# Kernel optimization log

Measured on AMD Instinct MI355X. Metric: run time of the kernel, lower is better.

## Reference

```python
import jax, jax.numpy as jnp
import numpy as np

N_HEAD = 16
LN_EPS = 1e-5     # torch LayerNorm default
ATTN_EPS = 1e-6   # fast-transformers CausalLinearAttention eps


def layer_norm(x, g, b):
    mu = x.mean(-1, keepdims=True)
    var = ((x - mu) ** 2).mean(-1, keepdims=True)
    return (x - mu) * jax.lax.rsqrt(var + LN_EPS) * g + b


def favor(x, omega):
    # Favor/Performer softmax-kernel features.
    # x: [B,S,H,dh], omega: [dh, m/2] -> phi: [B,S,H,m] with m = 2*(dh//2) = dh
    dh = x.shape[-1]
    m = 2 * omega.shape[-1]
    xs = x * (dh ** -0.25)  # x * sqrt(softmax_temp), softmax_temp = 1/sqrt(dh)
    u = jnp.einsum('bshd,dm->bshm', xs, omega)
    h = 0.5 * jnp.sum(xs * xs, axis=-1, keepdims=True)  # ||x||^2 / 2
    return jnp.concatenate([jnp.exp(u - h), jnp.exp(-u - h)], axis=-1) * (m ** -0.5)


def causal_linear_attention(q, k, v):
    # q,k: [B,S,H,M] feature-mapped; v: [B,S,H,Dv]
    # out[i] = (phiQ_i @ sum_{j<=i} phiK_j v_j^T) / (phiQ_i . sum_{j<=i} phiK_j)
    B, S, H, M = q.shape
    Dv = v.shape[-1]
    qT = jnp.moveaxis(q, 1, 0)  # [S,B,H,M]
    kT = jnp.moveaxis(k, 1, 0)
    vT = jnp.moveaxis(v, 1, 0)  # [S,B,H,Dv]
    S0 = jnp.zeros((B, H, M, Dv), q.dtype)
    z0 = jnp.zeros((B, H, M), q.dtype)

    def step(carry, qkv):
        Sst, zst = carry
        qi, ki, vi = qkv
        Sst = Sst + ki[..., :, None] * vi[..., None, :]  # [B,H,M,Dv]
        zst = zst + ki                                   # [B,H,M]
        num = jnp.einsum('bhm,bhmd->bhd', qi, Sst)
        den = jnp.einsum('bhm,bhm->bh', qi, zst) + ATTN_EPS
        return (Sst, zst), num / den[..., None]

    _, out = jax.lax.scan(step, (S0, z0), (qT, kT, vT))
    return jnp.moveaxis(out, 0, 1)  # [B,S,H,Dv]


def forward(x, Wq, bq, Wk, bk, Wv, bv, Wo, bo, omega,
            ln1_g, ln1_b, ln2_g, ln2_b, W1, bf1, W2, bf2):
    L = Wq.shape[0]
    B, S, D = x.shape
    dh = D // N_HEAD
    out = x
    for l in range(L):  # fixed small layer count
        q = (out @ Wq[l] + bq[l]).reshape(B, S, N_HEAD, dh)
        k = (out @ Wk[l] + bk[l]).reshape(B, S, N_HEAD, dh)
        v = (out @ Wv[l] + bv[l]).reshape(B, S, N_HEAD, dh)
        Qf = favor(q, omega[l])
        Kf = favor(k, omega[l])
        a = causal_linear_attention(Qf, Kf, v).reshape(B, S, D)
        a = a @ Wo[l] + bo[l]
        h = layer_norm(out + a, ln1_g[l], ln1_b[l])          # norm1 (post-norm)
        y = jax.nn.relu(h @ W1[l] + bf1[l]) @ W2[l] + bf2[l]  # FFN
        out = layer_norm(h + y, ln2_g[l], ln2_b[l])          # norm2
    return out


def setup_inputs() -> dict:
    key = jax.random.key(0)
    L, B, S, D, DFF = 3, 2, 1024, 1024, 4096
    dh = D // N_HEAD
    ks = jax.random.split(key, 8)
    g = lambda k, shape: jax.random.normal(k, shape, jnp.float32) * 0.02
    return {
        'x': jax.random.normal(ks[0], (B, S, D), jnp.float32),
        'Wq': g(ks[1], (L, D, D)), 'bq': jnp.zeros((L, D), jnp.float32),
        'Wk': g(ks[2], (L, D, D)), 'bk': jnp.zeros((L, D), jnp.float32),
        'Wv': g(ks[3], (L, D, D)), 'bv': jnp.zeros((L, D), jnp.float32),
        'Wo': g(ks[4], (L, D, D)), 'bo': jnp.zeros((L, D), jnp.float32),
        'omega': jax.random.normal(ks[5], (L, dh, dh // 2), jnp.float32),
        'ln1_g': jnp.ones((L, D), jnp.float32), 'ln1_b': jnp.zeros((L, D), jnp.float32),
        'ln2_g': jnp.ones((L, D), jnp.float32), 'ln2_b': jnp.zeros((L, D), jnp.float32),
        'W1': g(ks[6], (L, D, DFF)), 'bf1': jnp.zeros((L, DFF), jnp.float32),
        'W2': g(ks[7], (L, DFF, D)), 'bf2': jnp.zeros((L, D), jnp.float32),
    }


def reference(x, Wq, bq, Wk, bk, Wv, bv, Wo, bo, omega,
              ln1_g, ln1_b, ln2_g, ln2_b, W1, bf1, W2, bf2):
    return forward(x, Wq, bq, Wk, bk, Wv, bv, Wo, bo, omega,
                   ln1_g, ln1_b, ln2_g, ln2_b, W1, bf1, W2, bf2)
```

## Files before the change

### kernel.cpp

```cpp
#include <hip/hip_runtime.h>

typedef unsigned int u32;
typedef unsigned short u16;
typedef unsigned long long u64;

#define LN_EPS 1e-5f
#define ATTN_EPS 1e-6f

typedef __bf16 bf16x8 __attribute__((ext_vector_type(8)));
typedef short shortx8 __attribute__((ext_vector_type(8)));
typedef float fx4 __attribute__((ext_vector_type(4)));

__device__ __forceinline__ u16 f2bf(float f){
  union{float f; u32 u;} x; x.f = f;
  u32 r = 0x7fffu + ((x.u>>16)&1u);
  return (u16)((x.u + r)>>16);
}
__device__ __forceinline__ float bf2f(u16 u){
  union{u32 u; float f;} x; x.u = ((u32)u)<<16; return x.f;
}
__device__ __forceinline__ bf16x8 ldfrag(const u16* p){
  return __builtin_bit_cast(bf16x8, *(const shortx8*)p);
}

__device__ __forceinline__ void async16(const void* g, void* l){
  typedef const __attribute__((address_space(1))) void gas_t;
  typedef __attribute__((address_space(3))) void las_t;
  __builtin_amdgcn_global_load_lds((gas_t*)(u64)g, (las_t*)(u32)(u64)l, 16, 0, 0);
}

__global__ void detect_kernel(const u16* __restrict__ ln1g, int* __restrict__ flag){
  if (threadIdx.x == 0 && blockIdx.x == 0)
    *flag = (ln1g[0] == 0x3F80u) ? 1 : 0;
}

__global__ __launch_bounds__(256) void cvt_small(
    const void* p0, const void* p1, const void* p2, const void* p3,
    const void* p4, const void* p5, const void* p6, const void* p7,
    const void* p8, const void* p9, const void* p10,
    float* __restrict__ out, const int* __restrict__ flagp)
{
  int i = blockIdx.x*256 + threadIdx.x;
  if (i >= 46080) return;
  const void* src; int off;
  if      (i < 3072)  { src=p0;  off=i; }
  else if (i < 6144)  { src=p1;  off=i-3072; }
  else if (i < 9216)  { src=p2;  off=i-6144; }
  else if (i < 12288) { src=p3;  off=i-9216; }
  else if (i < 18432) { src=p4;  off=i-12288; }
  else if (i < 21504) { src=p5;  off=i-18432; }
  else if (i < 24576) { src=p6;  off=i-21504; }
  else if (i < 27648) { src=p7;  off=i-24576; }
  else if (i < 30720) { src=p8;  off=i-27648; }
  else if (i < 43008) { src=p9;  off=i-30720; }
  else                { src=p10; off=i-43008; }
  float v;
  if (*flagp){ union{u32 u; float f;} x; x.u = ((u32)((const u16*)src)[off])<<16; v = x.f; }
  else v = ((const float*)src)[off];
  out[i] = v;
}

__global__ __launch_bounds__(256) void cvt_x(const void* __restrict__ in, float* __restrict__ out,
                                             u16* __restrict__ outbf, int n, const int* __restrict__ flagp){
  int i = blockIdx.x*256 + threadIdx.x;
  if (i >= n) return;
  float v;
  if (*flagp){ union{u32 u; float f;} x; x.u = ((u32)((const u16*)in)[i])<<16; v = x.f; }
  else v = ((const float*)in)[i];
  out[i] = v;
  outbf[i] = f2bf(v);
}

__global__ __launch_bounds__(256) void transpose_cvt(
    const void* __restrict__ W, size_t eoff, u16* __restrict__ Wt,
    int K, int N, const int* __restrict__ flagp)
{
  __shared__ float s[32][33];
  const int bx = blockIdx.x, by = blockIdx.y;
  const int tid = threadIdx.x;
  const int c = tid & 31, r = tid >> 5;
  const int isbf = *flagp;
#pragma unroll
  for (int i = 0; i < 4; ++i){
    int k = by*32 + r + i*8, n = bx*32 + c;
    size_t idx = eoff + (size_t)k*N + n;
    float v;
    if (isbf){ union{u32 u; float f;} x; x.u = ((u32)((const u16*)W)[idx])<<16; v = x.f; }
    else v = ((const float*)W)[idx];
    s[r + i*8][c] = v;
  }
  __syncthreads();
#pragma unroll
  for (int i = 0; i < 4; ++i){
    int n = bx*32 + r + i*8, k = by*32 + c;
    Wt[(size_t)n*K + k] = f2bf(s[c][r + i*8]);
  }
}

__global__ __launch_bounds__(256) void transpose_cvt4(
    const void* __restrict__ W0, const void* __restrict__ W1,
    const void* __restrict__ W2, const void* __restrict__ W3,
    size_t eoff, u16* __restrict__ Wt, size_t wtz,
    int K, int N, const int* __restrict__ flagp)
{
  __shared__ float s[32][33];
  const int z = blockIdx.z;
  const void* W = (z==0)?W0:((z==1)?W1:((z==2)?W2:W3));
  Wt += (size_t)z * wtz;
  const int bx = blockIdx.x, by = blockIdx.y;
  const int tid = threadIdx.x;
  const int c = tid & 31, r = tid >> 5;
  const int isbf = *flagp;
#pragma unroll
  for (int i = 0; i < 4; ++i){
    int k = by*32 + r + i*8, n = bx*32 + c;
    size_t idx = eoff + (size_t)k*N + n;
    float v;
    if (isbf){ union{u32 u; float f;} x; x.u = ((u32)((const u16*)W)[idx])<<16; v = x.f; }
    else v = ((const float*)W)[idx];
    s[r + i*8][c] = v;
  }
  __syncthreads();
#pragma unroll
  for (int i = 0; i < 4; ++i){
    int n = bx*32 + r + i*8, k = by*32 + c;
    Wt[(size_t)n*K + k] = f2bf(s[c][r + i*8]);
  }
}

__global__ __launch_bounds__(256, 1) void mfma_gemm(
    const u16* __restrict__ A, const u16* __restrict__ W,
    const float* __restrict__ bias,
    float* __restrict__ C, u16* __restrict__ Cbf,
    int N, int Kst, int kstep_z, int klen,
    size_t wz, size_t cz, int bz, int bias_all, int relu)
{
  __shared__ u16 As[3][128*32];
  __shared__ u16 Bs[3][128*32];
  const int z = blockIdx.z;
  W    += (size_t)z * wz;
  bias += (size_t)z * bz;
  if (C) C += (size_t)z * cz;
  const int kbeg = z * kstep_z;
  const int tid = threadIdx.x;
  const int lane = tid & 63, wid = tid >> 6;
  const int row0 = blockIdx.y * 128, col0 = blockIdx.x * 128;

  const int ar0 = tid >> 2,        ae0 = (tid & 3) << 3;
  const int ar1 = (256+tid) >> 2,  ae1 = (tid & 3) << 3;
  const u16* gA0 = A + (size_t)(row0 + ar0)*Kst + kbeg + ae0;
  const u16* gA1 = A + (size_t)(row0 + ar1)*Kst + kbeg + ae1;
  const u16* gB0 = W + (size_t)(col0 + ar0)*Kst + kbeg + ae0;
  const u16* gB1 = W + (size_t)(col0 + ar1)*Kst + kbeg + ae1;

  const int iters = klen >> 5;
#pragma unroll
  for (int s = 0; s < 2; ++s){
    const int ko = s*32;
    async16(gA0 + ko, &As[s][tid*8]);
    async16(gA1 + ko, &As[s][2048 + tid*8]);
    async16(gB0 + ko, &Bs[s][tid*8]);
    async16(gB1 + ko, &Bs[s][2048 + tid*8]);
  }

  const int quad = lane >> 4, l16 = lane & 15;
  const int wr = (wid >> 1) * 64, wc = (wid & 1) * 64;
  fx4 acc[4][4] = {};

  for (int it = 0; it < iters; ++it){
    const int cur = it % 3;
    __builtin_amdgcn_s_waitcnt(0x0F74);
    __builtin_amdgcn_s_barrier();
    {
      const int nx   = (it + 2 < iters) ? (it + 2) : (iters - 1);
      const int nbuf = (it + 2) % 3;
      const int ko = nx*32;
      async16(gA0 + ko, &As[nbuf][tid*8]);
      async16(gA1 + ko, &As[nbuf][2048 + tid*8]);
      async16(gB0 + ko, &Bs[nbuf][tid*8]);
      async16(gB1 + ko, &Bs[nbuf][2048 + tid*8]);
    }
    bf16x8 af[4], bfr[4];
#pragma unroll
    for (int t = 0; t < 4; ++t)
      af[t] = ldfrag(&As[cur][(wr + t*16 + l16)*32 + quad*8]);
#pragma unroll
    for (int u = 0; u < 4; ++u)
      bfr[u] = ldfrag(&Bs[cur][(wc + u*16 + l16)*32 + quad*8]);
#pragma unroll
    for (int t = 0; t < 4; ++t)
#pragma unroll
      for (int u = 0; u < 4; ++u)
        acc[t][u] = __builtin_amdgcn_mfma_f32_16x16x32_bf16(af[t], bfr[u], acc[t][u], 0, 0, 0);
  }
  __builtin_amdgcn_s_waitcnt(0x0F70);

  const int r0 = quad * 4;
#pragma unroll
  for (int u = 0; u < 4; ++u){
    const int col = col0 + wc + u*16 + l16;
    const float bv = (bias_all || z == 0) ? bias[col] : 0.f;
#pragma unroll
    for (int t = 0; t < 4; ++t){
      const int rowb = row0 + wr + t*16 + r0;
#pragma unroll
      for (int r = 0; r < 4; ++r){
        float v = acc[t][u][r] + bv;
        if (relu) v = fmaxf(v, 0.f);
        if (C)   C[(size_t)(rowb + r)*N + col] = v;
        if (Cbf) Cbf[(size_t)(rowb + r)*N + col] = f2bf(v);
      }
    }
  }
}

__global__ __launch_bounds__(256) void favor_kernel(
    float* __restrict__ Q, float* __restrict__ Kp, const float* __restrict__ omega,
    u16* __restrict__ Qb, u16* __restrict__ Kb)
{
  __shared__ float sh[4][64];
  __shared__ float sho[64][32];
  int tid = threadIdx.x;
  for (int i = tid; i < 2048; i += 256)
    sho[i>>5][i&31] = omega[i];
  int wv = tid >> 6, lane = tid & 63;
  int th = blockIdx.x*4 + wv;
  size_t base = (size_t)(th >> 4) * 1024 + (size_t)(th & 15) * 64;
  int jm = lane & 31;
  float sgn = (lane < 32) ? 1.f : -1.f;
  for (int w = 0; w < 2; ++w){
    float* p = w ? Kp : Q;
    float xs = p[base + lane] * 0.35355339059327373f;
    __syncthreads();
    sh[wv][lane] = xs;
    __syncthreads();
    float u = 0.f, hh = 0.f;
#pragma unroll
    for (int d = 0; d < 64; ++d){
      float xv = sh[wv][d];
      u  = fmaf(xv, sho[d][jm], u);
      hh = fmaf(xv, xv, hh);
    }
    float phi = expf(sgn*u - 0.5f*hh) * 0.125f;
    if (w) p[base + lane] = phi;
    (w ? Kb : Qb)[base + lane] = f2bf(phi);
  }
}

__global__ __launch_bounds__(256) void chunk_kv(
    const float* __restrict__ Kf, const float* __restrict__ V,
    float* __restrict__ KV, float* __restrict__ Ksum)
{
  __shared__ float Ks[64][64];
  __shared__ float Vs[64][64];
  int blk = blockIdx.x;
  int c = blk & 15, h = (blk >> 4) & 15, b = blk >> 8;
  int tid = threadIdx.x;
  for (int i = tid; i < 1024; i += 256){
    int j = i >> 4, m4 = (i & 15) << 2;
    size_t src = ((size_t)(b*1024 + c*64 + j)*16 + h)*64 + m4;
    *(float4*)&Ks[j][m4] = *(const float4*)&Kf[src];
    *(float4*)&Vs[j][m4] = *(const float4*)&V[src];
  }
  __syncthreads();
  int m = tid & 63, dg = tid >> 6;
  float acc[16] = {0.f};
  for (int j = 0; j < 64; ++j){
    float kv = Ks[j][m];
#pragma unroll
    for (int di = 0; di < 16; ++di)
      acc[di] = fmaf(Vs[j][dg*16+di], kv, acc[di]);
  }
  size_t outb = (size_t)blk * 4096;
#pragma unroll
  for (int di = 0; di < 16; ++di)
    KV[outb + (size_t)(dg*16+di)*64 + m] = acc[di];
  if (tid < 64){
    float s = 0.f;
    for (int j = 0; j < 64; ++j) s += Ks[j][tid];
    Ksum[(size_t)blk*64 + tid] = s;
  }
}

__global__ __launch_bounds__(256) void chunk_scan(float* __restrict__ KV, float* __restrict__ Ksum)
{
  int blk = blockIdx.x;
  int bh = blk >> 4, ec = blk & 15;
  int e = ec*256 + threadIdx.x;
  size_t base = (size_t)bh * 65536 + e;
  float run = 0.f;
  for (int c = 0; c < 16; ++c){
    size_t idx = base + (size_t)c*4096;
    float t = KV[idx]; KV[idx] = run; run += t;
  }
  if (ec == 0 && threadIdx.x < 64){
    size_t kb = (size_t)bh * 1024 + threadIdx.x;
    float rz = 0.f;
    for (int c = 0; c < 16; ++c){
      size_t idx = kb + c*64;
      float t = Ksum[idx]; Ksum[idx] = rz; rz += t;
    }
  }
}

__global__ __launch_bounds__(256) void attn_kernel(
    const u16* __restrict__ Qbf, const u16* __restrict__ Kbf,
    const float* __restrict__ V, const float* __restrict__ KVt,
    const float* __restrict__ Ksum, u16* __restrict__ Outbf)
{
  __shared__ u16 Qs[64][72];
  __shared__ u16 Ks[64][72];
  __shared__ u16 Ss[64][72];
  __shared__ u16 Vt[64][72];
  __shared__ u16 Pt[64][72];
  __shared__ float Vrow[64][68];
  __shared__ float densum[64];

  const int blk = blockIdx.x;
  const int c = blk & 15, h = (blk >> 4) & 15, b = blk >> 8;
  const int tid = threadIdx.x;
  const int lane = tid & 63, w = tid >> 6;
  const int quad = lane >> 4, l16 = lane & 15;
  const int t0 = b*1024 + c*64;

  {
    const int r = tid >> 2, q4 = (tid & 3) << 4;
    size_t g = (size_t)(t0 + r)*1024 + h*64 + q4;
    *(uint4*)&Qs[r][q4]   = *(const uint4*)(Qbf + g);
    *(uint4*)&Qs[r][q4+8] = *(const uint4*)(Qbf + g + 8);
    *(uint4*)&Ks[r][q4]   = *(const uint4*)(Kbf + g);
    *(uint4*)&Ks[r][q4+8] = *(const uint4*)(Kbf + g + 8);
    const float* vg = V + g;
    *(float4*)&Vrow[r][q4+0]  = *(const float4*)(vg+0);
    *(float4*)&Vrow[r][q4+4]  = *(const float4*)(vg+4);
    *(float4*)&Vrow[r][q4+8]  = *(const float4*)(vg+8);
    *(float4*)&Vrow[r][q4+12] = *(const float4*)(vg+12);
    const float* pg = KVt + (size_t)blk*4096 + r*64 + q4;
    u16 tmp[16];
#pragma unroll
    for (int j = 0; j < 16; ++j) tmp[j] = f2bf(pg[j]);
    *(uint4*)&Pt[r][q4]   = *(uint4*)&tmp[0];
    *(uint4*)&Pt[r][q4+8] = *(uint4*)&tmp[8];
  }
  __syncthreads();
  {
    const int d = tid >> 2, j16 = (tid & 3) << 4;
    u16 tmp[16];
#pragma unroll
    for (int j = 0; j < 16; ++j) tmp[j] = f2bf(Vrow[j16+j][d]);
    *(uint4*)&Vt[d][j16]   = *(uint4*)&tmp[0];
    *(uint4*)&Vt[d][j16+8] = *(uint4*)&tmp[8];
  }

  const int iw0 = w*16;
  bf16x8 aq0 = ldfrag(&Qs[iw0+l16][quad*8]);
  bf16x8 aq1 = ldfrag(&Qs[iw0+l16][32+quad*8]);
  fx4 sacc[4];
#pragma unroll
  for (int u = 0; u < 4; ++u){
    sacc[u] = (fx4){0.f,0.f,0.f,0.f};
    bf16x8 b0 = ldfrag(&Ks[u*16+l16][quad*8]);
    bf16x8 b1 = ldfrag(&Ks[u*16+l16][32+quad*8]);
    sacc[u] = __builtin_amdgcn_mfma_f32_16x16x32_bf16(aq0, b0, sacc[u], 0, 0, 0);
    sacc[u] = __builtin_amdgcn_mfma_f32_16x16x32_bf16(aq1, b1, sacc[u], 0, 0, 0);
  }
  float rs[4] = {0.f,0.f,0.f,0.f};
#pragma unroll
  for (int u = 0; u < 4; ++u){
    const int jl = u*16 + l16;
#pragma unroll
    for (int r = 0; r < 4; ++r){
      const int il = iw0 + quad*4 + r;
      float v = (jl <= il) ? sacc[u][r] : 0.f;
      rs[r] += v;
      Ss[il][jl] = f2bf(v);
    }
  }
#pragma unroll
  for (int off = 1; off < 16; off <<= 1){
#pragma unroll
    for (int r = 0; r < 4; ++r) rs[r] += __shfl_xor(rs[r], off);
  }
  if (l16 == 0){
#pragma unroll
    for (int r = 0; r < 4; ++r) densum[iw0 + quad*4 + r] = rs[r];
  }
  __syncthreads();

  {
    const int row = iw0 + l16;
    const float* zp = Ksum + (size_t)blk*64;
    float dp = 0.f;
#pragma unroll
    for (int m = 0; m < 16; ++m){
      const int mm = quad*16 + m;
      dp = fmaf(bf2f(Qs[row][mm]), zp[mm], dp);
    }
    dp += __shfl_xor(dp, 16);
    dp += __shfl_xor(dp, 32);
    if (quad == 0) densum[row] = densum[row] + dp + ATTN_EPS;
  }
  __syncthreads();

  bf16x8 as0 = ldfrag(&Ss[iw0+l16][quad*8]);
  bf16x8 as1 = ldfrag(&Ss[iw0+l16][32+quad*8]);
  fx4 oacc[4];
#pragma unroll
  for (int u = 0; u < 4; ++u){
    const int d0 = u*16;
    oacc[u] = (fx4){0.f,0.f,0.f,0.f};
    oacc[u] = __builtin_amdgcn_mfma_f32_16x16x32_bf16(as0, ldfrag(&Vt[d0+l16][quad*8]),    oacc[u], 0,0,0);
    oacc[u] = __builtin_amdgcn_mfma_f32_16x16x32_bf16(as1, ldfrag(&Vt[d0+l16][32+quad*8]), oacc[u], 0,0,0);
    oacc[u] = __builtin_amdgcn_mfma_f32_16x16x32_bf16(aq0, ldfrag(&Pt[d0+l16][quad*8]),    oacc[u], 0,0,0);
    oacc[u] = __builtin_amdgcn_mfma_f32_16x16x32_bf16(aq1, ldfrag(&Pt[d0+l16][32+quad*8]), oacc[u], 0,0,0);
  }
#pragma unroll
  for (int u = 0; u < 4; ++u){
    const int d = u*16 + l16;
#pragma unroll
    for (int r = 0; r < 4; ++r){
      const int il = iw0 + quad*4 + r;
      const float o = oacc[u][r] / densum[il];
      Outbf[(size_t)(t0 + il)*1024 + h*64 + d] = f2bf(o);
    }
  }
}

__global__ __launch_bounds__(256) void resid_ln(
    const float* __restrict__ X, const float* __restrict__ Y0, const float* __restrict__ Y1,
    const float* __restrict__ g, const float* __restrict__ b,
    float* __restrict__ Dst, u16* __restrict__ DstBf,
    void* __restrict__ OutPtr, const int* __restrict__ flagp)
{
  __shared__ float rs[4], rss[4];
  int row = blockIdx.x, tid = threadIdx.x;
  int lane = tid & 63, wv = tid >> 6;
  size_t base = (size_t)row * 1024;
  int c = tid << 2;
  float4 xv = *(const float4*)&X[base + c];
  float4 y0 = *(const float4*)&Y0[base + c];
  float4 y1 = *(const float4*)&Y1[base + c];
  float v0 = xv.x+y0.x+y1.x, v1 = xv.y+y0.y+y1.y, v2 = xv.z+y0.z+y1.z, v3 = xv.w+y0.w+y1.w;
  float s = v0+v1+v2+v3;
  float ss = v0*v0+v1*v1+v2*v2+v3*v3;
  for (int off = 32; off; off >>= 1){
    s  += __shfl_down(s, off);
    ss += __shfl_down(ss, off);
  }
  if (lane == 0){ rs[wv] = s; rss[wv] = ss; }
  __syncthreads();
  float S  = rs[0]+rs[1]+rs[2]+rs[3];
  float SS = rss[0]+rss[1]+rss[2]+rss[3];
  float mu = S * (1.f/1024.f);
  float var = SS * (1.f/1024.f) - mu*mu;
  float rinv = rsqrtf(var + LN_EPS);
  float4 gv = *(const float4*)(g + c);
  float4 bb = *(const float4*)(b + c);
  float o0 = (v0-mu)*rinv*gv.x + bb.x;
  float o1 = (v1-mu)*rinv*gv.y + bb.y;
  float o2 = (v2-mu)*rinv*gv.z + bb.z;
  float o3 = (v3-mu)*rinv*gv.w + bb.w;
  *(float4*)&Dst[base + c] = make_float4(o0,o1,o2,o3);
  uint2 ob;
  ob.x = (u32)f2bf(o0) | ((u32)f2bf(o1) << 16);
  ob.y = (u32)f2bf(o2) | ((u32)f2bf(o3) << 16);
  *(uint2*)(DstBf + base + c) = ob;
  if (OutPtr){
    if (*flagp){
      *(uint2*)((u16*)OutPtr + base + c) = ob;
    } else {
      *(float4*)((float*)OutPtr + base + c) = make_float4(o0,o1,o2,o3);
    }
  }
}

extern "C" void kernel_launch(void* const* d_in, const int* in_sizes, int n_in,
                              void* d_out, int out_size, void* d_ws, size_t ws_size,
                              hipStream_t stream)
{
  (void)in_sizes; (void)n_in; (void)out_size; (void)ws_size;

  float* ws   = (float*)d_ws;
  float* bufA = ws;
  float* bufQ = bufA + 2097152;
  float* bufK = bufQ + 2097152;
  float* bufV = bufK + 2097152;
  float* KV   = bufV + 2097152;
  float* Ks   = KV   + 2097152;
  float* smallP = Ks + 32768;
  float* pend = smallP + 46080;
  int* flag = (int*)pend;
  u16* abf  = (u16*)(pend + 4);
  u16* hbf  = abf  + 2097152;
  u16* t1bf = hbf  + 2097152;
  u16* fbf  = t1bf + 2097152;
  u16* Wt   = fbf  + 8388608;
  u16* qpbf = Wt   + 4194304;
  u16* kpbf = qpbf + 2097152;

  float* bqF  = smallP + 0;
  float* boF  = smallP + 9216;
  float* omF  = smallP + 12288;
  float* l1gF = smallP + 18432;
  float* l1bF = smallP + 21504;
  float* l2gF = smallP + 24576;
  float* l2bF = smallP + 27648;
  float* bf1F = smallP + 30720;
  float* bf2F = smallP + 43008;

  detect_kernel<<<1, 64, 0, stream>>>((const u16*)d_in[10], flag);
  cvt_small<<<180, 256, 0, stream>>>(d_in[2], d_in[4], d_in[6], d_in[8], d_in[9],
                                     d_in[10], d_in[11], d_in[12], d_in[13],
                                     d_in[15], d_in[17], smallP, flag);
  cvt_x<<<8192, 256, 0, stream>>>(d_in[0], bufA, abf, 2097152, flag);

  dim3 tQKVO(32, 32, 4);
  dim3 tF1(128, 32);
  dim3 tF2(32, 128);
  dim3 gQKV(8, 16, 3);
  dim3 gO(8, 16, 2);
  dim3 gF1(32, 16, 1);
  dim3 gF2(8, 16, 2);

  for (int l = 0; l < 3; ++l){
    size_t offD = (size_t)l * 1048576;
    size_t offF = (size_t)l * 4194304;

    transpose_cvt4<<<tQKVO, 256, 0, stream>>>(d_in[1], d_in[3], d_in[5], d_in[7],
                                              offD, Wt, 1048576, 1024, 1024, flag);

    mfma_gemm<<<gQKV, 256, 0, stream>>>(abf, Wt, bqF + l*1024, bufQ, (u16*)nullptr,
                                        1024, 1024, 0, 1024,
                                        1048576, 2097152, 3072, 1, 0);
    favor_kernel<<<8192, 256, 0, stream>>>(bufQ, bufK, omF + l*2048, qpbf, kpbf);
    chunk_kv<<<512, 256, 0, stream>>>(bufK, bufV, KV, Ks);
    chunk_scan<<<512, 256, 0, stream>>>(KV, Ks);
    attn_kernel<<<512, 256, 0, stream>>>(qpbf, kpbf, bufV, KV, Ks, t1bf);

    mfma_gemm<<<gO, 256, 0, stream>>>(t1bf, Wt + 3145728, boF + l*1024, bufQ, (u16*)nullptr,
                                      1024, 1024, 512, 512,
                                      0, 4194304, 0, 0, 0);
    resid_ln<<<2048, 256, 0, stream>>>(bufA, bufQ, bufV, l1gF + l*1024, l1bF + l*1024,
                                       bufK, hbf, nullptr, flag);

    transpose_cvt<<<tF1, 256, 0, stream>>>(d_in[14], offF, Wt, 1024, 4096, flag);
    mfma_gemm<<<gF1, 256, 0, stream>>>(hbf, Wt, bf1F + l*4096, (float*)nullptr, fbf,
                                       4096, 1024, 0, 1024,
                                       0, 0, 0, 1, 1);

    transpose_cvt<<<tF2, 256, 0, stream>>>(d_in[16], offF, Wt, 4096, 1024, flag);
    mfma_gemm<<<gF2, 256, 0, stream>>>(fbf, Wt, bf2F + l*1024, bufQ, (u16*)nullptr,
                                       1024, 4096, 2048, 2048,
                                       0, 4194304, 0, 0, 0);

    resid_ln<<<2048, 256, 0, stream>>>(bufK, bufQ, bufV, l2gF + l*1024, l2bF + l*1024,
                                       bufA, abf, (l == 2) ? d_out : nullptr, flag);
  }
}
```

Before: 800.4 us.

## Deepen GEMM pipeline, remap blocks across XCDs, split-K by four for O/FFN2

The GEMM's shared-memory ring grows from three to four stages, with prefetch three tiles ahead and a matching waitcnt. Block indices are remapped so neighbouring column tiles spread across the eight XCDs. The output and FFN2 GEMMs now split K four ways into a new partial buffer, and the residual LayerNorm sums all four partials. This aims to hide more load latency and put more blocks on the device, at the cost of more shared memory per block and extra partial-buffer traffic.

Result: slower. 856.3 us (+7.0%).

```diff
diff --git a/kernel.cpp b/kernel.cpp
--- a/kernel.cpp
+++ b/kernel.cpp
@@ -135,8 +135,8 @@
     int N, int Kst, int kstep_z, int klen,
     size_t wz, size_t cz, int bz, int bias_all, int relu)
 {
-  __shared__ u16 As[3][128*32];
-  __shared__ u16 Bs[3][128*32];
+  __shared__ u16 As[4][128*32];
+  __shared__ u16 Bs[4][128*32];
   const int z = blockIdx.z;
   W    += (size_t)z * wz;
   bias += (size_t)z * bz;
@@ -144,7 +144,11 @@
   const int kbeg = z * kstep_z;
   const int tid = threadIdx.x;
   const int lane = tid & 63, wid = tid >> 6;
-  const int row0 = blockIdx.y * 128, col0 = blockIdx.x * 128;
+
+  const int flat = blockIdx.y * gridDim.x + blockIdx.x;
+  const int xcd = flat & 7, sblk = flat >> 3;
+  const int by = sblk & 15, bxs = (sblk >> 4) * 8 + xcd;
+  const int row0 = by * 128, col0 = bxs * 128;
 
   const int ar0 = tid >> 2,        ae0 = (tid & 3) << 3;
   const int ar1 = (256+tid) >> 2,  ae1 = (tid & 3) << 3;
@@ -155,7 +159,7 @@
 
   const int iters = klen >> 5;
 #pragma unroll
-  for (int s = 0; s < 2; ++s){
+  for (int s = 0; s < 3; ++s){
     const int ko = s*32;
     async16(gA0 + ko, &As[s][tid*8]);
     async16(gA1 + ko, &As[s][2048 + tid*8]);
@@ -168,12 +172,12 @@
   fx4 acc[4][4] = {};
 
   for (int it = 0; it < iters; ++it){
-    const int cur = it % 3;
-    __builtin_amdgcn_s_waitcnt(0x0F74);
+    const int cur = it & 3;
+    __builtin_amdgcn_s_waitcnt(0x0F78);
     __builtin_amdgcn_s_barrier();
     {
-      const int nx   = (it + 2 < iters) ? (it + 2) : (iters - 1);
-      const int nbuf = (it + 2) % 3;
+      const int nx   = (it + 3 < iters) ? (it + 3) : (iters - 1);
+      const int nbuf = (it + 3) & 3;
       const int ko = nx*32;
       async16(gA0 + ko, &As[nbuf][tid*8]);
       async16(gA1 + ko, &As[nbuf][2048 + tid*8]);
@@ -427,7 +431,9 @@
 }
 
 __global__ __launch_bounds__(256) void resid_ln(
-    const float* __restrict__ X, const float* __restrict__ Y0, const float* __restrict__ Y1,
+    const float* __restrict__ X,
+    const float* __restrict__ Y0, const float* __restrict__ Y1,
+    const float* __restrict__ Y2, const float* __restrict__ Y3,
     const float* __restrict__ g, const float* __restrict__ b,
     float* __restrict__ Dst, u16* __restrict__ DstBf,
     void* __restrict__ OutPtr, const int* __restrict__ flagp)
@@ -440,7 +446,12 @@
   float4 xv = *(const float4*)&X[base + c];
   float4 y0 = *(const float4*)&Y0[base + c];
   float4 y1 = *(const float4*)&Y1[base + c];
-  float v0 = xv.x+y0.x+y1.x, v1 = xv.y+y0.y+y1.y, v2 = xv.z+y0.z+y1.z, v3 = xv.w+y0.w+y1.w;
+  float4 y2 = *(const float4*)&Y2[base + c];
+  float4 y3 = *(const float4*)&Y3[base + c];
+  float v0 = xv.x+y0.x+y1.x+y2.x+y3.x;
+  float v1 = xv.y+y0.y+y1.y+y2.y+y3.y;
+  float v2 = xv.z+y0.z+y1.z+y2.z+y3.z;
+  float v3 = xv.w+y0.w+y1.w+y2.w+y3.w;
   float s = v0+v1+v2+v3;
   float ss = v0*v0+v1*v1+v2*v2+v3*v3;
   for (int off = 32; off; off >>= 1){
@@ -497,6 +508,7 @@
   u16* Wt   = fbf  + 8388608;
   u16* qpbf = Wt   + 4194304;
   u16* kpbf = qpbf + 2097152;
+  float* part = (float*)(kpbf + 2097152);
 
   float* bqF  = smallP + 0;
   float* boF  = smallP + 9216;
@@ -518,9 +530,9 @@
   dim3 tF1(128, 32);
   dim3 tF2(32, 128);
   dim3 gQKV(8, 16, 3);
-  dim3 gO(8, 16, 2);
+  dim3 gO(8, 16, 4);
   dim3 gF1(32, 16, 1);
-  dim3 gF2(8, 16, 2);
+  dim3 gF2(8, 16, 4);
 
   for (int l = 0; l < 3; ++l){
     size_t offD = (size_t)l * 1048576;
@@ -537,10 +549,11 @@
     chunk_scan<<<512, 256, 0, stream>>>(KV, Ks);
     attn_kernel<<<512, 256, 0, stream>>>(qpbf, kpbf, bufV, KV, Ks, t1bf);
 
-    mfma_gemm<<<gO, 256, 0, stream>>>(t1bf, Wt + 3145728, boF + l*1024, bufQ, (u16*)nullptr,
-                                      1024, 1024, 512, 512,
-                                      0, 4194304, 0, 0, 0);
-    resid_ln<<<2048, 256, 0, stream>>>(bufA, bufQ, bufV, l1gF + l*1024, l1bF + l*1024,
+    mfma_gemm<<<gO, 256, 0, stream>>>(t1bf, Wt + 3145728, boF + l*1024, part, (u16*)nullptr,
+                                      1024, 1024, 256, 256,
+                                      0, 2097152, 0, 0, 0);
+    resid_ln<<<2048, 256, 0, stream>>>(bufA, part, part + 2097152, part + 4194304, part + 6291456,
+                                       l1gF + l*1024, l1bF + l*1024,
                                        bufK, hbf, nullptr, flag);
 
     transpose_cvt<<<tF1, 256, 0, stream>>>(d_in[14], offF, Wt, 1024, 4096, flag);
@@ -549,11 +562,12 @@
                                        0, 0, 0, 1, 1);
 
     transpose_cvt<<<tF2, 256, 0, stream>>>(d_in[16], offF, Wt, 4096, 1024, flag);
-    mfma_gemm<<<gF2, 256, 0, stream>>>(fbf, Wt, bf2F + l*1024, bufQ, (u16*)nullptr,
-                                       1024, 4096, 2048, 2048,
-                                       0, 4194304, 0, 0, 0);
-
-    resid_ln<<<2048, 256, 0, stream>>>(bufK, bufQ, bufV, l2gF + l*1024, l2bF + l*1024,
+    mfma_gemm<<<gF2, 256, 0, stream>>>(fbf, Wt, bf2F + l*1024, part, (u16*)nullptr,
+                                       1024, 4096, 1024, 1024,
+                                       0, 2097152, 0, 0, 0);
+
+    resid_ln<<<2048, 256, 0, stream>>>(bufK, part, part + 2097152, part + 4194304, part + 6291456,
+                                       l2gF + l*1024, l2bF + l*1024,
                                        bufA, abf, (l == 2) ? d_out : nullptr, flag);
   }
 }
```

## Store QKV in bf16, deepen GEMM pipeline to four stages, swizzle blocks across XCDs

Applied to the files above, without the earlier changes.

The QKV projection GEMM now writes bf16 instead of fp32. The favor, chunk_kv and attention kernels read those bf16 Q/K/V buffers, and chunk_kv takes its K features from the bf16 phi buffer instead of an fp32 copy. This cuts intermediate memory traffic and drops the fp32 rewrite of K features. Separately, the MFMA GEMM moves from a 3-buffer to a 4-buffer LDS pipeline with three tiles in flight, and remaps block indices so neighbouring tiles are spread across the eight XCDs. The trade-offs are lower precision for Q/K/V and the K features used in the KV state, plus double the LDS per GEMM block.

Measured after the change: 801.1 us. No clear change (+0.1%).

```diff
diff --git a/kernel.cpp b/kernel.cpp
--- a/kernel.cpp
+++ b/kernel.cpp
@@ -133,18 +133,23 @@
     const float* __restrict__ bias,
     float* __restrict__ C, u16* __restrict__ Cbf,
     int N, int Kst, int kstep_z, int klen,
-    size_t wz, size_t cz, int bz, int bias_all, int relu)
-{
-  __shared__ u16 As[3][128*32];
-  __shared__ u16 Bs[3][128*32];
+    size_t wz, size_t cz, size_t cbz, int bz, int bias_all, int relu)
+{
+  __shared__ u16 As[4][128*32];
+  __shared__ u16 Bs[4][128*32];
   const int z = blockIdx.z;
   W    += (size_t)z * wz;
   bias += (size_t)z * bz;
-  if (C) C += (size_t)z * cz;
+  if (C)   C   += (size_t)z * cz;
+  if (Cbf) Cbf += (size_t)z * cbz;
   const int kbeg = z * kstep_z;
   const int tid = threadIdx.x;
   const int lane = tid & 63, wid = tid >> 6;
-  const int row0 = blockIdx.y * 128, col0 = blockIdx.x * 128;
+
+  const int flat = blockIdx.y * gridDim.x + blockIdx.x;
+  const int xcd = flat & 7, sblk = flat >> 3;
+  const int by = sblk & 15, bxs = (sblk >> 4) * 8 + xcd;
+  const int row0 = by * 128, col0 = bxs * 128;
 
   const int ar0 = tid >> 2,        ae0 = (tid & 3) << 3;
   const int ar1 = (256+tid) >> 2,  ae1 = (tid & 3) << 3;
@@ -155,7 +160,7 @@
 
   const int iters = klen >> 5;
 #pragma unroll
-  for (int s = 0; s < 2; ++s){
+  for (int s = 0; s < 3; ++s){
     const int ko = s*32;
     async16(gA0 + ko, &As[s][tid*8]);
     async16(gA1 + ko, &As[s][2048 + tid*8]);
@@ -168,12 +173,12 @@
   fx4 acc[4][4] = {};
 
   for (int it = 0; it < iters; ++it){
-    const int cur = it % 3;
-    __builtin_amdgcn_s_waitcnt(0x0F74);
+    const int cur = it & 3;
+    __builtin_amdgcn_s_waitcnt(0x0F78);
     __builtin_amdgcn_s_barrier();
     {
-      const int nx   = (it + 2 < iters) ? (it + 2) : (iters - 1);
-      const int nbuf = (it + 2) % 3;
+      const int nx   = (it + 3 < iters) ? (it + 3) : (iters - 1);
+      const int nbuf = (it + 3) & 3;
       const int ko = nx*32;
       async16(gA0 + ko, &As[nbuf][tid*8]);
       async16(gA1 + ko, &As[nbuf][2048 + tid*8]);
@@ -215,8 +220,9 @@
 }
 
 __global__ __launch_bounds__(256) void favor_kernel(
-    float* __restrict__ Q, float* __restrict__ Kp, const float* __restrict__ omega,
-    u16* __restrict__ Qb, u16* __restrict__ Kb)
+    const u16* __restrict__ Qin, const u16* __restrict__ Kin,
+    const float* __restrict__ omega,
+    u16* __restrict__ Qphi, u16* __restrict__ Kphi)
 {
   __shared__ float sh[4][64];
   __shared__ float sho[64][32];
@@ -229,8 +235,8 @@
   int jm = lane & 31;
   float sgn = (lane < 32) ? 1.f : -1.f;
   for (int w = 0; w < 2; ++w){
-    float* p = w ? Kp : Q;
-    float xs = p[base + lane] * 0.35355339059327373f;
+    const u16* p = w ? Kin : Qin;
+    float xs = bf2f(p[base + lane]) * 0.35355339059327373f;
     __syncthreads();
     sh[wv][lane] = xs;
     __syncthreads();
@@ -242,13 +248,12 @@
       hh = fmaf(xv, xv, hh);
     }
     float phi = expf(sgn*u - 0.5f*hh) * 0.125f;
-    if (w) p[base + lane] = phi;
-    (w ? Kb : Qb)[base + lane] = f2bf(phi);
+    (w ? Kphi : Qphi)[base + lane] = f2bf(phi);
   }
 }
 
 __global__ __launch_bounds__(256) void chunk_kv(
-    const float* __restrict__ Kf, const float* __restrict__ V,
+    const u16* __restrict__ Kf, const u16* __restrict__ V,
     float* __restrict__ KV, float* __restrict__ Ksum)
 {
   __shared__ float Ks[64][64];
@@ -259,8 +264,12 @@
   for (int i = tid; i < 1024; i += 256){
     int j = i >> 4, m4 = (i & 15) << 2;
     size_t src = ((size_t)(b*1024 + c*64 + j)*16 + h)*64 + m4;
-    *(float4*)&Ks[j][m4] = *(const float4*)&Kf[src];
-    *(float4*)&Vs[j][m4] = *(const float4*)&V[src];
+    uint2 kk = *(const uint2*)(Kf + src);
+    uint2 vv = *(const uint2*)(V + src);
+    Ks[j][m4+0] = bf2f((u16)kk.x); Ks[j][m4+1] = bf2f((u16)(kk.x>>16));
+    Ks[j][m4+2] = bf2f((u16)kk.y); Ks[j][m4+3] = bf2f((u16)(kk.y>>16));
+    Vs[j][m4+0] = bf2f((u16)vv.x); Vs[j][m4+1] = bf2f((u16)(vv.x>>16));
+    Vs[j][m4+2] = bf2f((u16)vv.y); Vs[j][m4+3] = bf2f((u16)(vv.y>>16));
   }
   __syncthreads();
   int m = tid & 63, dg = tid >> 6;
@@ -305,15 +314,15 @@
 
 __global__ __launch_bounds__(256) void attn_kernel(
     const u16* __restrict__ Qbf, const u16* __restrict__ Kbf,
-    const float* __restrict__ V, const float* __restrict__ KVt,
+    const u16* __restrict__ V, const float* __restrict__ KVt,
     const float* __restrict__ Ksum, u16* __restrict__ Outbf)
 {
   __shared__ u16 Qs[64][72];
   __shared__ u16 Ks[64][72];
   __shared__ u16 Ss[64][72];
+  __shared__ u16 Vb[64][72];
   __shared__ u16 Vt[64][72];
   __shared__ u16 Pt[64][72];
-  __shared__ float Vrow[64][68];
   __shared__ float densum[64];
 
   const int blk = blockIdx.x;
@@ -330,11 +339,8 @@
     *(uint4*)&Qs[r][q4+8] = *(const uint4*)(Qbf + g + 8);
     *(uint4*)&Ks[r][q4]   = *(const uint4*)(Kbf + g);
     *(uint4*)&Ks[r][q4+8] = *(const uint4*)(Kbf + g + 8);
-    const float* vg = V + g;
-    *(float4*)&Vrow[r][q4+0]  = *(const float4*)(vg+0);
-    *(float4*)&Vrow[r][q4+4]  = *(const float4*)(vg+4);
-    *(float4*)&Vrow[r][q4+8]  = *(const float4*)(vg+8);
-    *(float4*)&Vrow[r][q4+12] = *(const float4*)(vg+12);
+    *(uint4*)&Vb[r][q4]   = *(const uint4*)(V + g);
+    *(uint4*)&Vb[r][q4+8] = *(const uint4*)(V + g + 8);
     const float* pg = KVt + (size_t)blk*4096 + r*64 + q4;
     u16 tmp[16];
 #pragma unroll
@@ -347,7 +353,7 @@
     const int d = tid >> 2, j16 = (tid & 3) << 4;
     u16 tmp[16];
 #pragma unroll
-    for (int j = 0; j < 16; ++j) tmp[j] = f2bf(Vrow[j16+j][d]);
+    for (int j = 0; j < 16; ++j) tmp[j] = Vb[j16+j][d];
     *(uint4*)&Vt[d][j16]   = *(uint4*)&tmp[0];
     *(uint4*)&Vt[d][j16+8] = *(uint4*)&tmp[8];
   }
@@ -427,7 +433,8 @@
 }
 
 __global__ __launch_bounds__(256) void resid_ln(
-    const float* __restrict__ X, const float* __restrict__ Y0, const float* __restrict__ Y1,
+    const float* __restrict__ X,
+    const float* __restrict__ Y0, const float* __restrict__ Y1,
     const float* __restrict__ g, const float* __restrict__ b,
     float* __restrict__ Dst, u16* __restrict__ DstBf,
     void* __restrict__ OutPtr, const int* __restrict__ flagp)
@@ -495,7 +502,8 @@
   u16* t1bf = hbf  + 2097152;
   u16* fbf  = t1bf + 2097152;
   u16* Wt   = fbf  + 8388608;
-  u16* qpbf = Wt   + 4194304;
+  u16* qkvb = Wt   + 4194304;
+  u16* qpbf = qkvb + 6291456;
   u16* kpbf = qpbf + 2097152;
 
   float* bqF  = smallP + 0;
@@ -529,29 +537,29 @@
     transpose_cvt4<<<tQKVO, 256, 0, stream>>>(d_in[1], d_in[3], d_in[5], d_in[7],
                                               offD, Wt, 1048576, 1024, 1024, flag);
 
-    mfma_gemm<<<gQKV, 256, 0, stream>>>(abf, Wt, bqF + l*1024, bufQ, (u16*)nullptr,
+    mfma_gemm<<<gQKV, 256, 0, stream>>>(abf, Wt, bqF + l*1024, (float*)nullptr, qkvb,
                                         1024, 1024, 0, 1024,
-                                        1048576, 2097152, 3072, 1, 0);
-    favor_kernel<<<8192, 256, 0, stream>>>(bufQ, bufK, omF + l*2048, qpbf, kpbf);
-    chunk_kv<<<512, 256, 0, stream>>>(bufK, bufV, KV, Ks);
+                                        1048576, 0, 2097152, 3072, 1, 0);
+    favor_kernel<<<8192, 256, 0, stream>>>(qkvb, qkvb + 2097152, omF + l*2048, qpbf, kpbf);
+    chunk_kv<<<512, 256, 0, stream>>>(kpbf, qkvb + 4194304, KV, Ks);
     chunk_scan<<<512, 256, 0, stream>>>(KV, Ks);
-    attn_kernel<<<512, 256, 0, stream>>>(qpbf, kpbf, bufV, KV, Ks, t1bf);
+    attn_kernel<<<512, 256, 0, stream>>>(qpbf, kpbf, qkvb + 4194304, KV, Ks, t1bf);
 
     mfma_gemm<<<gO, 256, 0, stream>>>(t1bf, Wt + 3145728, boF + l*1024, bufQ, (u16*)nullptr,
                                       1024, 1024, 512, 512,
-                                      0, 4194304, 0, 0, 0);
+                                      0, 4194304, 0, 0, 0, 0);
     resid_ln<<<2048, 256, 0, stream>>>(bufA, bufQ, bufV, l1gF + l*1024, l1bF + l*1024,
                                        bufK, hbf, nullptr, flag);
 
     transpose_cvt<<<tF1, 256, 0, stream>>>(d_in[14], offF, Wt, 1024, 4096, flag);
     mfma_gemm<<<gF1, 256, 0, stream>>>(hbf, Wt, bf1F + l*4096, (float*)nullptr, fbf,
                                        4096, 1024, 0, 1024,
-                                       0, 0, 0, 1, 1);
+                                       0, 0, 0, 0, 1, 1);
 
     transpose_cvt<<<tF2, 256, 0, stream>>>(d_in[16], offF, Wt, 4096, 1024, flag);
     mfma_gemm<<<gF2, 256, 0, stream>>>(fbf, Wt, bf2F + l*1024, bufQ, (u16*)nullptr,
                                        1024, 4096, 2048, 2048,
-                                       0, 4194304, 0, 0, 0);
+                                       0, 4194304, 0, 0, 0, 0);
 
     resid_ln<<<2048, 256, 0, stream>>>(bufK, bufQ, bufV, l2gF + l*1024, l2bF + l*1024,
                                        bufA, abf, (l == 2) ? d_out : nullptr, flag);
```
